# Optimization experiments

Measured on AMD Instinct MI355X. Metric: run time of the kernel, lower is better.

Reference implementation:

```python
import jax, jax.numpy as jnp
import numpy as np

INPUT_SIZE = 21
HIDDEN = 50
OUTPUT = 24
BATCH = 4096
SEQ = 336


def setup_inputs() -> dict:
    key = jax.random.key(0)
    ks = jax.random.split(key, 7)
    s_ih = 1.0 / np.sqrt(HIDDEN)
    x = jax.random.normal(ks[0], (BATCH, SEQ, INPUT_SIZE), dtype=jnp.float32)
    # PyTorch LSTM params: gate order i, f, g, o stacked along dim0
    W_ih = jax.random.uniform(ks[1], (4 * HIDDEN, INPUT_SIZE), minval=-s_ih, maxval=s_ih, dtype=jnp.float32)
    W_hh = jax.random.uniform(ks[2], (4 * HIDDEN, HIDDEN), minval=-s_ih, maxval=s_ih, dtype=jnp.float32)
    b_ih = jax.random.uniform(ks[3], (4 * HIDDEN,), minval=-s_ih, maxval=s_ih, dtype=jnp.float32)
    b_hh = jax.random.uniform(ks[4], (4 * HIDDEN,), minval=-s_ih, maxval=s_ih, dtype=jnp.float32)
    s_fc = 1.0 / np.sqrt(HIDDEN)
    W_fc = jax.random.uniform(ks[5], (OUTPUT, HIDDEN), minval=-s_fc, maxval=s_fc, dtype=jnp.float32)
    b_fc = jax.random.uniform(ks[6], (OUTPUT,), minval=-s_fc, maxval=s_fc, dtype=jnp.float32)
    return {"x": x, "W_ih": W_ih, "W_hh": W_hh, "b_ih": b_ih, "b_hh": b_hh, "W_fc": W_fc, "b_fc": b_fc}


def _lstm_last(x, W_ih, W_hh, b_ih, b_hh):
    B = x.shape[0]
    H = W_hh.shape[1]
    # Precompute input projections for all timesteps: [T, B, 4H]
    x_proj = jnp.einsum('bti,gi->tbg', x, W_ih) + (b_ih + b_hh)

    def step(carry, xp):
        h, c = carry
        gates = xp + h @ W_hh.T  # [B, 4H]
        i_g, f_g, g_g, o_g = jnp.split(gates, 4, axis=-1)
        i_g = jax.nn.sigmoid(i_g)
        f_g = jax.nn.sigmoid(f_g)
        g_g = jnp.tanh(g_g)
        o_g = jax.nn.sigmoid(o_g)
        c = f_g * c + i_g * g_g
        h = o_g * jnp.tanh(c)
        return (h, c), None

    h0 = jnp.zeros((B, H), dtype=x.dtype)
    c0 = jnp.zeros((B, H), dtype=x.dtype)
    (h_last, _), _ = jax.lax.scan(step, (h0, c0), x_proj)
    return h_last


def reference(x, W_ih, W_hh, b_ih, b_hh, W_fc, b_fc):
    h_last = _lstm_last(x, W_ih, W_hh, b_ih, b_hh)  # [B, H]
    return h_last @ W_fc.T + b_fc  # [B, OUTPUT]
```

## Files before the change

kernel.cpp:

```cpp
#include <hip/hip_runtime.h>


#define T_SEQ 336
#define I_IN  21
#define HID   50
#define O_OUT 24
#define MB    16
#define NT    832
#define NTILE 13
#define CH    12
#define NCH   28
#define XELEM (CH * MB * I_IN)
#define NLD   5
#define XBUFH (CH * 4 * 16 * 8)

#define HIDX(buf, kb, n, j) ((((buf)*8 + (kb))*16 + (n))*8 + (j))
#define XIDX(s, kb, n, j)   ((((s)*4 + (kb))*16 + (n))*8 + (j))

typedef _Float16 f16x8 __attribute__((ext_vector_type(8)));
typedef float    f32x4 __attribute__((ext_vector_type(4)));

static __device__ __forceinline__ float frcp(float v) { return __builtin_amdgcn_rcpf(v); }
static __device__ __forceinline__ float sigm(float v) { return frcp(1.f + __expf(-v)); }
static __device__ __forceinline__ float tanh_f(float v) {
    return __builtin_fmaf(-2.f, frcp(1.f + __expf(2.f * v)), 1.f);
}

__global__ __launch_bounds__(NT)
void lstm_mfma8(const float* __restrict__ x,
                const float* __restrict__ W_ih,
                const float* __restrict__ W_hh,
                const float* __restrict__ b_ih,
                const float* __restrict__ b_hh,
                const float* __restrict__ W_fc,
                const float* __restrict__ b_fc,
                float* __restrict__ out)
{
    __shared__ _Float16 hbuf[2 * 8 * 16 * 8];
    __shared__ _Float16 xC[2 * XBUFH];

    const int tid  = threadIdx.x;
    const int lane = tid & 63;
    const int wv   = tid >> 6;
    const int nl   = lane & 15;
    const int q    = lane >> 4;
    const int b0   = blockIdx.x * MB;

    for (int i = tid; i < 2 * 8 * 16 * 8; i += NT) hbuf[i] = (_Float16)0.f;
    for (int i = tid; i < 2 * XBUFH;      i += NT) xC[i]   = (_Float16)0.f;

    const float* px[NLD];
    int  xdst[NLD];
    bool xv[NLD];
    float sv[NLD];
    #pragma unroll
    for (int k = 0; k < NLD; ++k) {
        const int e  = tid + k * NT;
        const int i  = e % I_IN;
        const int r  = e / I_IN;
        const int b  = r & 15;
        const int sI = r >> 4;
        xv[k]   = (e < XELEM);
        px[k]   = x + ((size_t)(b0 + b) * T_SEQ + sI) * I_IN + i;
        xdst[k] = XIDX(sI, i >> 3, b, i & 7);
        sv[k]   = px[k][0];
    }

    f16x8 Wh[3], Wl[3];
    f32x4 biasv;
    {
        const int p    = wv * 16 + nl;
        const int unit = p >> 2, gate = p & 3;
        const bool vr  = (unit < HID);
        const int orig = gate * HID + unit;
        const int ub   = wv * 4 + q;
        #pragma unroll
        for (int r = 0; r < 4; ++r)
            biasv[r] = (ub < HID) ? (b_ih[r * HID + ub] + b_hh[r * HID + ub]) : 0.f;
        #pragma unroll
        for (int kc = 0; kc < 3; ++kc) {
            #pragma unroll
            for (int j = 0; j < 8; ++j) {
                const int k = kc * 32 + q * 8 + j;
                float w = 0.f;
                if (vr) {
                    if (k < 64) { if (k < HID) w = W_hh[orig * HID + k]; }
                    else { const int ki = k - 64; if (ki < I_IN) w = W_ih[orig * I_IN + ki]; }
                }
                const _Float16 hi = (_Float16)w;
                Wh[kc][j] = hi;
                Wl[kc][j] = (_Float16)(w - (float)hi);
            }
        }
    }

    __syncthreads();

    #pragma unroll
    for (int k = 0; k < NLD; ++k) {
        if (xv[k]) xC[xdst[k]] = (_Float16)sv[k];
        px[k] += CH * I_IN;
    }

    const int  uown = wv * 4 + q;
    const bool uval = (uown < HID);
    const int  hwo  = ((uown >> 3) * 16 + nl) * 8 + (uown & 7);
    float cst = 0.f;

    const _Float16* hb0 = &hbuf[HIDX(0, q, nl, 0)];
    const int bfo = ((q * 16) + nl) * 8;

    for (int c = 0; c < NCH; ++c) {
        const int  rb    = (c & 1) * XBUFH;
        const int  wb    = ((c + 1) & 1) * XBUFH;
        const bool dostg = (c + 1) < NCH;
        #pragma unroll 2
        for (int s = 0; s < CH; ++s) {
            __syncthreads();

            if (s == 0 && dostg) {
                #pragma unroll
                for (int k = 0; k < NLD; ++k) sv[k] = px[k][0];
            }

            const int cur = s & 1, nxt = cur ^ 1;

            const _Float16* hb = hb0 + cur * 1024;
            const f16x8 B0 = *(const f16x8*)(hb);
            const f16x8 B1 = *(const f16x8*)(hb + 4 * 16 * 8);
            const f16x8 B2 = *(const f16x8*)&xC[rb + s * 512 + bfo];

            f32x4 aA = biasv;
            f32x4 aB = {0.f, 0.f, 0.f, 0.f};
            aA = __builtin_amdgcn_mfma_f32_16x16x32_f16(Wh[0], B0, aA, 0, 0, 0);
            aB = __builtin_amdgcn_mfma_f32_16x16x32_f16(Wl[0], B0, aB, 0, 0, 0);
            aA = __builtin_amdgcn_mfma_f32_16x16x32_f16(Wh[1], B1, aA, 0, 0, 0);
            aB = __builtin_amdgcn_mfma_f32_16x16x32_f16(Wl[1], B1, aB, 0, 0, 0);
            aA = __builtin_amdgcn_mfma_f32_16x16x32_f16(Wh[2], B2, aA, 0, 0, 0);
            aB = __builtin_amdgcn_mfma_f32_16x16x32_f16(Wl[2], B2, aB, 0, 0, 0);

            if (uval) {
                const float gi = aA[0] + aB[0];
                const float gf = aA[1] + aB[1];
                const float gg = aA[2] + aB[2];
                const float go = aA[3] + aB[3];
                float cc = cst;
                cc = __builtin_fmaf(sigm(gf), cc, sigm(gi) * tanh_f(gg));
                cst = cc;
                const float h = sigm(go) * tanh_f(cc);
                hbuf[nxt * 1024 + hwo] = (_Float16)h;
            }

            if (s == 0 && dostg) {
                #pragma unroll
                for (int k = 0; k < NLD; ++k) {
                    if (xv[k]) xC[wb + xdst[k]] = (_Float16)sv[k];
                    px[k] += CH * I_IN;
                }
            }
        }
    }

    __syncthreads();
    if (tid < MB * O_OUT) {
        const int b = tid / O_OUT, o = tid % O_OUT;
        float a = b_fc[o];
        for (int u = 0; u < HID; ++u) {
            const float hv = (float)hbuf[HIDX(0, u >> 3, b, u & 7)];
            a = __builtin_fmaf(hv, W_fc[o * HID + u], a);
        }
        out[(size_t)(b0 + b) * O_OUT + o] = a;
    }
}

extern "C" void kernel_launch(void* const* d_in, const int* in_sizes, int n_in,
                              void* d_out, int out_size, void* d_ws, size_t ws_size,
                              hipStream_t stream)
{
    const float* x    = (const float*)d_in[0];
    const float* W_ih = (const float*)d_in[1];
    const float* W_hh = (const float*)d_in[2];
    const float* b_ih = (const float*)d_in[3];
    const float* b_hh = (const float*)d_in[4];
    const float* W_fc = (const float*)d_in[5];
    const float* b_fc = (const float*)d_in[6];
    float* out = (float*)d_out;

    lstm_mfma8<<<dim3(4096 / MB), dim3(NT), 0, stream>>>(
        x, W_ih, W_hh, b_ih, b_hh, W_fc, b_fc, out);
}
```

Measured before the change: 325.8 us.

## Give each wave two gate tiles and fold exp2 scaling into weights

The block shrinks from 13 waves to 8, and each wave now computes two 16-row gate tiles with interleaved MFMA chains. This is meant to cut barrier and launch overhead and add instruction-level parallelism within a wave. Weights and biases are pre-scaled by -log2(e) or 2·log2(e), so the activations call exp2 directly and skip a multiply per gate. The x staging loop is widened to match the new thread count. The risks are higher register pressure and longer per-wave serial work on each recurrence step.

```diff
diff --git a/kernel.cpp b/kernel.cpp
--- a/kernel.cpp
+++ b/kernel.cpp
@@ -6,28 +6,31 @@
 #define HID   50
 #define O_OUT 24
 #define MB    16
-#define NT    832
-#define NTILE 13
+#define NT    512
+#define TPW   2
 #define CH    12
 #define NCH   28
 #define XELEM (CH * MB * I_IN)
-#define NLD   5
+#define NLD   8
 #define XBUFH (CH * 4 * 16 * 8)
 
 #define HIDX(buf, kb, n, j) ((((buf)*8 + (kb))*16 + (n))*8 + (j))
 #define XIDX(s, kb, n, j)   ((((s)*4 + (kb))*16 + (n))*8 + (j))
 
+#define K_LOG2E 1.44269504088896340736f
+
 typedef _Float16 f16x8 __attribute__((ext_vector_type(8)));
 typedef float    f32x4 __attribute__((ext_vector_type(4)));
 
 static __device__ __forceinline__ float frcp(float v) { return __builtin_amdgcn_rcpf(v); }
-static __device__ __forceinline__ float sigm(float v) { return frcp(1.f + __expf(-v)); }
-static __device__ __forceinline__ float tanh_f(float v) {
-    return __builtin_fmaf(-2.f, frcp(1.f + __expf(2.f * v)), 1.f);
+static __device__ __forceinline__ float ex2(float v)  { return __builtin_amdgcn_exp2f(v); }
+static __device__ __forceinline__ float sigm2(float g) { return frcp(1.f + ex2(g)); }
+static __device__ __forceinline__ float tanh2(float g) {
+    return __builtin_fmaf(-2.f, frcp(1.f + ex2(g)), 1.f);
 }
 
 __global__ __launch_bounds__(NT)
-void lstm_mfma8(const float* __restrict__ x,
+void lstm_mfma9(const float* __restrict__ x,
                 const float* __restrict__ W_ih,
                 const float* __restrict__ W_hh,
                 const float* __restrict__ b_ih,
@@ -66,17 +69,22 @@
         sv[k]   = px[k][0];
     }
 
-    f16x8 Wh[3], Wl[3];
-    f32x4 biasv;
-    {
-        const int p    = wv * 16 + nl;
+    f16x8 Wh[TPW][3], Wl[TPW][3];
+    f32x4 biasv[TPW];
+    #pragma unroll
+    for (int tt = 0; tt < TPW; ++tt) {
+        const int t    = wv * TPW + tt;
+        const int p    = t * 16 + nl;
         const int unit = p >> 2, gate = p & 3;
         const bool vr  = (unit < HID);
+        const float ws = (gate == 2) ? (2.f * K_LOG2E) : (-K_LOG2E);
         const int orig = gate * HID + unit;
-        const int ub   = wv * 4 + q;
+        const int ub   = t * 4 + q;
         #pragma unroll
-        for (int r = 0; r < 4; ++r)
-            biasv[r] = (ub < HID) ? (b_ih[r * HID + ub] + b_hh[r * HID + ub]) : 0.f;
+        for (int r = 0; r < 4; ++r) {
+            const float bs = (r == 2) ? (2.f * K_LOG2E) : (-K_LOG2E);
+            biasv[tt][r] = (ub < HID) ? (b_ih[r * HID + ub] + b_hh[r * HID + ub]) * bs : 0.f;
+        }
         #pragma unroll
         for (int kc = 0; kc < 3; ++kc) {
             #pragma unroll
@@ -87,9 +95,10 @@
                     if (k < 64) { if (k < HID) w = W_hh[orig * HID + k]; }
                     else { const int ki = k - 64; if (ki < I_IN) w = W_ih[orig * I_IN + ki]; }
                 }
+                w *= ws;
                 const _Float16 hi = (_Float16)w;
-                Wh[kc][j] = hi;
-                Wl[kc][j] = (_Float16)(w - (float)hi);
+                Wh[tt][kc][j] = hi;
+                Wl[tt][kc][j] = (_Float16)(w - (float)hi);
             }
         }
     }
@@ -102,10 +111,11 @@
         px[k] += CH * I_IN;
     }
 
-    const int  uown = wv * 4 + q;
-    const bool uval = (uown < HID);
-    const int  hwo  = ((uown >> 3) * 16 + nl) * 8 + (uown & 7);
-    float cst = 0.f;
+    const int u0 = (wv * TPW + 0) * 4 + q;
+    const int u1 = (wv * TPW + 1) * 4 + q;
+    const int hwo0 = ((u0 >> 3) * 16 + nl) * 8 + (u0 & 7);
+    const int hwo1 = ((u1 >> 3) * 16 + nl) * 8 + (u1 & 7);
+    float cst0 = 0.f, cst1 = 0.f;
 
     const _Float16* hb0 = &hbuf[HIDX(0, q, nl, 0)];
     const int bfo = ((q * 16) + nl) * 8;
@@ -130,25 +140,42 @@
             const f16x8 B1 = *(const f16x8*)(hb + 4 * 16 * 8);
             const f16x8 B2 = *(const f16x8*)&xC[rb + s * 512 + bfo];
 
-            f32x4 aA = biasv;
-            f32x4 aB = {0.f, 0.f, 0.f, 0.f};
-            aA = __builtin_amdgcn_mfma_f32_16x16x32_f16(Wh[0], B0, aA, 0, 0, 0);
-            aB = __builtin_amdgcn_mfma_f32_16x16x32_f16(Wl[0], B0, aB, 0, 0, 0);
-            aA = __builtin_amdgcn_mfma_f32_16x16x32_f16(Wh[1], B1, aA, 0, 0, 0);
-            aB = __builtin_amdgcn_mfma_f32_16x16x32_f16(Wl[1], B1, aB, 0, 0, 0);
-            aA = __builtin_amdgcn_mfma_f32_16x16x32_f16(Wh[2], B2, aA, 0, 0, 0);
-            aB = __builtin_amdgcn_mfma_f32_16x16x32_f16(Wl[2], B2, aB, 0, 0, 0);
-
-            if (uval) {
-                const float gi = aA[0] + aB[0];
-                const float gf = aA[1] + aB[1];
-                const float gg = aA[2] + aB[2];
-                const float go = aA[3] + aB[3];
-                float cc = cst;
-                cc = __builtin_fmaf(sigm(gf), cc, sigm(gi) * tanh_f(gg));
-                cst = cc;
-                const float h = sigm(go) * tanh_f(cc);
-                hbuf[nxt * 1024 + hwo] = (_Float16)h;
+            f32x4 aA0 = biasv[0];
+            f32x4 aB0 = {0.f, 0.f, 0.f, 0.f};
+            f32x4 aA1 = biasv[1];
+            f32x4 aB1 = {0.f, 0.f, 0.f, 0.f};
+            aA0 = __builtin_amdgcn_mfma_f32_16x16x32_f16(Wh[0][0], B0, aA0, 0, 0, 0);
+            aA1 = __builtin_amdgcn_mfma_f32_16x16x32_f16(Wh[1][0], B0, aA1, 0, 0, 0);
+            aB0 = __builtin_amdgcn_mfma_f32_16x16x32_f16(Wl[0][0], B0, aB0, 0, 0, 0);
+            aB1 = __builtin_amdgcn_mfma_f32_16x16x32_f16(Wl[1][0], B0, aB1, 0, 0, 0);
+            aA0 = __builtin_amdgcn_mfma_f32_16x16x32_f16(Wh[0][1], B1, aA0, 0, 0, 0);
+            aA1 = __builtin_amdgcn_mfma_f32_16x16x32_f16(Wh[1][1], B1, aA1, 0, 0, 0);
+            aB0 = __builtin_amdgcn_mfma_f32_16x16x32_f16(Wl[0][1], B1, aB0, 0, 0, 0);
+            aB1 = __builtin_amdgcn_mfma_f32_16x16x32_f16(Wl[1][1], B1, aB1, 0, 0, 0);
+            aA0 = __builtin_amdgcn_mfma_f32_16x16x32_f16(Wh[0][2], B2, aA0, 0, 0, 0);
+            aA1 = __builtin_amdgcn_mfma_f32_16x16x32_f16(Wh[1][2], B2, aA1, 0, 0, 0);
+            aB0 = __builtin_amdgcn_mfma_f32_16x16x32_f16(Wl[0][2], B2, aB0, 0, 0, 0);
+            aB1 = __builtin_amdgcn_mfma_f32_16x16x32_f16(Wl[1][2], B2, aB1, 0, 0, 0);
+
+            {
+                const float gi = aA0[0] + aB0[0];
+                const float gf = aA0[1] + aB0[1];
+                const float gg = aA0[2] + aB0[2];
+                const float go = aA0[3] + aB0[3];
+                const float cc = __builtin_fmaf(sigm2(gf), cst0, sigm2(gi) * tanh2(gg));
+                cst0 = cc;
+                const float h = sigm2(go) * tanh2(2.f * K_LOG2E * cc);
+                hbuf[nxt * 1024 + hwo0] = (_Float16)h;
+            }
+            {
+                const float gi = aA1[0] + aB1[0];
+                const float gf = aA1[1] + aB1[1];
+                const float gg = aA1[2] + aB1[2];
+                const float go = aA1[3] + aB1[3];
+                const float cc = __builtin_fmaf(sigm2(gf), cst1, sigm2(gi) * tanh2(gg));
+                cst1 = cc;
+                const float h = sigm2(go) * tanh2(2.f * K_LOG2E * cc);
+                hbuf[nxt * 1024 + hwo1] = (_Float16)h;
             }
 
             if (s == 0 && dostg) {
@@ -186,6 +213,6 @@
     const float* b_fc = (const float*)d_in[6];
     float* out = (float*)d_out;
 
-    lstm_mfma8<<<dim3(4096 / MB), dim3(NT), 0, stream>>>(
+    lstm_mfma9<<<dim3(4096 / MB), dim3(NT), 0, stream>>>(
         x, W_ih, W_hh, b_ih, b_hh, W_fc, b_fc, out);
 }
```

After: 321.2 us. About the same (-1.4%).
